# Kernel tuning notes

Hardware: AMD Instinct MI355X
Metric: run time of the kernel (lower is better)

Reference implementation:

```python
import jax, jax.numpy as jnp
import numpy as np

NUM_HEADS = 8
B, S, D = 4, 2048, 512


def setup_inputs() -> dict:
    key = jax.random.key(0)
    ks = jax.random.split(key, 12)
    scale = 1.0 / np.sqrt(D)
    return {
        "v": jax.random.normal(ks[0], (B, S, D), dtype=jnp.float32),
        "k": jax.random.normal(ks[1], (B, S, D), dtype=jnp.float32),
        "q": jax.random.normal(ks[2], (B, S, D), dtype=jnp.float32),
        "Wq": jax.random.normal(ks[3], (D, D), dtype=jnp.float32) * scale,
        "bq": jnp.zeros((D,), dtype=jnp.float32),
        "Wk": jax.random.normal(ks[4], (D, D), dtype=jnp.float32) * scale,
        "bk": jnp.zeros((D,), dtype=jnp.float32),
        "Wv": jax.random.normal(ks[5], (D, D), dtype=jnp.float32) * scale,
        "bv": jnp.zeros((D,), dtype=jnp.float32),
        "Wo": jax.random.normal(ks[6], (D, D), dtype=jnp.float32) * scale,
        "bo": jnp.zeros((D,), dtype=jnp.float32),
        "top_k": 32,
    }


def reference(v, k, q, Wq, bq, Wk, bk, Wv, bv, Wo, bo, top_k):
    dh = D // NUM_HEADS  # per-head depth

    def split_heads(x):  # [B,S,D] -> [B,H,S,dh]
        return x.reshape(B, -1, NUM_HEADS, dh).transpose(0, 2, 1, 3)

    qh = split_heads(q @ Wq + bq)
    kh = split_heads(k @ Wk + bk)
    vh = split_heads(v @ Wv + bv)

    logits = jnp.einsum('bhqd,bhkd->bhqk', qh, kh) / jnp.sqrt(jnp.float32(dh))
    w = jax.nn.softmax(logits, axis=-1)  # [B,H,S,S]

    num_keys = w.shape[-1]
    if top_k < num_keys:
        vals, idx = jax.lax.top_k(w, top_k)  # [B,H,S,top_k]
        bb = jnp.arange(B)[:, None, None, None]
        hh = jnp.arange(NUM_HEADS)[None, :, None, None]
        qq = jnp.arange(S)[None, None, :, None]
        sparse = jnp.zeros_like(w).at[bb, hh, qq, idx].set(vals)
        # tf.linalg.normalize(ord=1): divide by L1 norm along last axis
        w = sparse / jnp.sum(jnp.abs(sparse), axis=-1, keepdims=True)

    attn = jnp.einsum('bhqk,bhkd->bhqd', w, vh)  # [B,H,S,dh]
    concat = attn.transpose(0, 2, 1, 3).reshape(B, -1, D)
    out = concat @ Wo + bo
    return (out, w)
```

## Files before the change

kernel.cpp:

```cpp
#include <hip/hip_runtime.h>
#include <hip/hip_bf16.h>
#include <stdint.h>

#define S_LEN 2048
#define DMODEL 512
#define NH 8
#define DH 64
#define TOPK 32
#define LO_SCALE 4096.0f
#define INV_LO (1.0f/4096.0f)

typedef _Float16 f16;
typedef f16 half8 __attribute__((ext_vector_type(8)));
typedef f16 half4 __attribute__((ext_vector_type(4)));
typedef float floatx4 __attribute__((ext_vector_type(4)));
typedef float f32x4 __attribute__((ext_vector_type(4)));
typedef unsigned long long u64k;

#define AS1 __attribute__((address_space(1)))
#define AS3 __attribute__((address_space(3)))

__device__ __forceinline__ void gl_lds16(const void* g, void* l) {
    __builtin_amdgcn_global_load_lds((const AS1 void*)g, (AS3 void*)l, 16, 0, 0);
}
__device__ __forceinline__ void lds_fence() {
    asm volatile("s_waitcnt lgkmcnt(0)" ::: "memory");
}

__device__ __forceinline__ u64k make_key(float f, int idx) {
    unsigned u = __float_as_uint(f);
    unsigned sv = u ^ ((unsigned)(((int)u) >> 31) | 0x80000000u);
    return ((u64k)sv << 16) | (u64k)(0xFFFFu - (unsigned)idx);
}

__global__ __launch_bounds__(256)
void qkproj(const float* __restrict__ Xq, const float* __restrict__ Xk,
            const float* __restrict__ Wq_, const float* __restrict__ Wk_,
            const float* __restrict__ bq_, const float* __restrict__ bk_,
            float* __restrict__ outQ, float* __restrict__ outK)
{
    __shared__ float As[32][132];
    __shared__ float Bs[32][132];
    const float* X    = blockIdx.z ? Xk  : Xq;
    const float* W    = blockIdx.z ? Wk_ : Wq_;
    const float* bias = blockIdx.z ? bk_ : bq_;
    float* out        = blockIdx.z ? outK : outQ;
    const int tid = threadIdx.x;
    const int tx = tid & 15;
    const int ty = tid >> 4;
    const int m0 = blockIdx.y * 128;
    const int n0 = blockIdx.x * 128;

    float acc[8][8];
#pragma unroll
    for (int i = 0; i < 8; ++i)
#pragma unroll
        for (int j = 0; j < 8; ++j) acc[i][j] = 0.f;

    f32x4 pa[4], pb[4];
#pragma unroll
    for (int u = 0; u < 4; ++u) {
        int id = tid + u * 256;
        pa[u] = *(const f32x4*)(X + (size_t)(m0 + (id >> 3)) * 512 + (id & 7) * 4);
        pb[u] = *(const f32x4*)(W + (size_t)(id >> 5) * 512 + n0 + (id & 31) * 4);
    }

    for (int k0 = 0; k0 < 512; k0 += 32) {
#pragma unroll
        for (int u = 0; u < 4; ++u) {
            int id = tid + u * 256;
            int r = id >> 3, c4 = (id & 7) * 4;
            As[c4 + 0][r] = pa[u].x; As[c4 + 1][r] = pa[u].y;
            As[c4 + 2][r] = pa[u].z; As[c4 + 3][r] = pa[u].w;
            int rb = id >> 5, cb = (id & 31) * 4;
            *(f32x4*)&Bs[rb][cb] = pb[u];
        }
        __syncthreads();
        if (k0 < 480) {
            int kn = k0 + 32;
#pragma unroll
            for (int u = 0; u < 4; ++u) {
                int id = tid + u * 256;
                pa[u] = *(const f32x4*)(X + (size_t)(m0 + (id >> 3)) * 512 + kn + (id & 7) * 4);
                pb[u] = *(const f32x4*)(W + (size_t)(kn + (id >> 5)) * 512 + n0 + (id & 31) * 4);
            }
        }
#pragma unroll 8
        for (int kk = 0; kk < 32; ++kk) {
            float a[8], b[8];
            *(f32x4*)&a[0] = *(const f32x4*)&As[kk][ty * 4];
            *(f32x4*)&a[4] = *(const f32x4*)&As[kk][64 + ty * 4];
            *(f32x4*)&b[0] = *(const f32x4*)&Bs[kk][tx * 4];
            *(f32x4*)&b[4] = *(const f32x4*)&Bs[kk][64 + tx * 4];
#pragma unroll
            for (int i = 0; i < 8; ++i)
#pragma unroll
                for (int j = 0; j < 8; ++j)
                    acc[i][j] = fmaf(a[i], b[j], acc[i][j]);
        }
        __syncthreads();
    }

    float bb[8];
    *(f32x4*)&bb[0] = *(const f32x4*)(bias + n0 + tx * 4);
    *(f32x4*)&bb[4] = *(const f32x4*)(bias + n0 + 64 + tx * 4);

#pragma unroll
    for (int i = 0; i < 8; ++i) {
        int r = m0 + ((i >> 2) << 6) + ty * 4 + (i & 3);
        int b_ = r >> 11, s = r & 2047;
#pragma unroll
        for (int h = 0; h < 2; ++h) {
            int c = n0 + h * 64 + tx * 4;
            f32x4 w = {acc[i][h * 4 + 0] + bb[h * 4 + 0],
                       acc[i][h * 4 + 1] + bb[h * 4 + 1],
                       acc[i][h * 4 + 2] + bb[h * 4 + 2],
                       acc[i][h * 4 + 3] + bb[h * 4 + 3]};
            int hd = c >> 6, d = c & 63;
            float* p = out + (((size_t)(b_ * NH + hd) * S_LEN) + s) * DH + d;
            *(f32x4*)p = w;
        }
    }
}

__global__ __launch_bounds__(256)
void logits_topk(const float* __restrict__ Qh, const float* __restrict__ Kh,
                 float* __restrict__ wbuf)
{
    __shared__ float As[2][32][68];
    __shared__ __align__(16) char smemB[33280];
    float* Bs = (float*)smemB;
    u64k (*slab)[32] = (u64k(*)[32])smemB;

    const int tid = threadIdx.x;
    const int lig = tid & 15;
    const int ty  = tid >> 4;
    const int gsh = ((tid & 63) >> 4) << 4;
    const unsigned ltg = (1u << lig) - 1u;
    const int bh = blockIdx.y;
    const int q0 = blockIdx.x * 64;
    const float* Ab = Qh + (size_t)bh * S_LEN * DH;
    const float* Bb = Kh + (size_t)bh * S_LEN * DH;

    auto sort32 = [&](u64k &a0, u64k &a1) {
#pragma unroll
        for (int s = 2; s <= 32; s <<= 1) {
#pragma unroll
            for (int d = s >> 1; d >= 1; d >>= 1) {
                int e0 = 2 * lig;
                if (d == 1) {
                    bool descB = ((e0 & s) == 0);
                    u64k mx = a0 > a1 ? a0 : a1;
                    u64k mn = a0 > a1 ? a1 : a0;
                    a0 = descB ? mx : mn;
                    a1 = descB ? mn : mx;
                } else {
                    bool descB = ((e0 & s) == 0);
                    bool amS   = ((e0 & d) == 0);
                    bool wantMax = (descB == amS);
                    u64k p0 = __shfl_xor(a0, d >> 1, 16);
                    u64k p1 = __shfl_xor(a1, d >> 1, 16);
                    a0 = wantMax ? (a0 > p0 ? a0 : p0) : (a0 > p0 ? p0 : a0);
                    a1 = wantMax ? (a1 > p1 ? a1 : p1) : (a1 > p1 ? p1 : a1);
                }
            }
        }
    };
    auto clean32 = [&](u64k &a0, u64k &a1) {
#pragma unroll
        for (int d = 16; d >= 2; d >>= 1) {
            bool amS = (((2 * lig) & d) == 0);
            u64k p0 = __shfl_xor(a0, d >> 1, 16);
            u64k p1 = __shfl_xor(a1, d >> 1, 16);
            a0 = amS ? (a0 > p0 ? a0 : p0) : (a0 > p0 ? p0 : a0);
            a1 = amS ? (a1 > p1 ? a1 : p1) : (a1 > p1 ? p1 : a1);
        }
        u64k mx = a0 > a1 ? a0 : a1;
        u64k mn = a0 > a1 ? a1 : a0;
        a0 = mx; a1 = mn;
    };

    float acc[4][16];
#pragma unroll
    for (int i = 0; i < 4; ++i)
#pragma unroll
        for (int j = 0; j < 16; ++j) acc[i][j] = 0.f;

    u64k key0[4], key1[4], botk[4];
#pragma unroll
    for (int i = 0; i < 4; ++i) { key0[i] = 0; key1[i] = 0; botk[i] = 0; }

#pragma unroll
    for (int u = 0; u < 4; ++u) {
        int id = tid + u * 256;
        int r = id >> 4, c4 = (id & 15) * 4;
        int ch = c4 >> 5, cl = c4 & 31;
        f32x4 x = *(const f32x4*)(Ab + (size_t)(q0 + r) * DH + c4);
        As[ch][cl + 0][r] = x.x * 0.125f;
        As[ch][cl + 1][r] = x.y * 0.125f;
        As[ch][cl + 2][r] = x.z * 0.125f;
        As[ch][cl + 3][r] = x.w * 0.125f;
    }

    f32x4 kb[8];
#pragma unroll
    for (int u = 0; u < 8; ++u) {
        int id = tid + u * 256;
        int r = id >> 3, c4 = (id & 7) * 4;
        kb[u] = *(const f32x4*)(Bb + (size_t)r * DH + c4);
    }

#pragma unroll 1
    for (int kp = 0; kp < 8; ++kp) {
#pragma unroll
        for (int ch = 0; ch < 2; ++ch) {
            __syncthreads();
#pragma unroll
            for (int u = 0; u < 8; ++u) {
                int id = tid + u * 256;
                int r = id >> 3, c4 = (id & 7) * 4;
                Bs[(c4 + 0) * 260 + r] = kb[u].x;
                Bs[(c4 + 1) * 260 + r] = kb[u].y;
                Bs[(c4 + 2) * 260 + r] = kb[u].z;
                Bs[(c4 + 3) * 260 + r] = kb[u].w;
            }
            __syncthreads();
            {
                int nkp = ch ? kp + 1 : kp;
                int nch = ch ^ 1;
                if (nkp < 8) {
#pragma unroll
                    for (int u = 0; u < 8; ++u) {
                        int id = tid + u * 256;
                        int r = id >> 3, c4 = (id & 7) * 4;
                        kb[u] = *(const f32x4*)(Bb + (size_t)(nkp * 256 + r) * DH + nch * 32 + c4);
                    }
                }
            }
#pragma unroll 8
            for (int kk = 0; kk < 32; ++kk) {
                float a[4], b[16];
                *(f32x4*)&a[0] = *(const f32x4*)&As[ch][kk][ty * 4];
#pragma unroll
                for (int h = 0; h < 4; ++h)
                    *(f32x4*)&b[h * 4] = *(const f32x4*)&Bs[kk * 260 + lig * 4 + h * 64];
#pragma unroll
                for (int i = 0; i < 4; ++i)
#pragma unroll
                    for (int j = 0; j < 16; ++j)
                        acc[i][j] = fmaf(a[i], b[j], acc[i][j]);
            }
        }
        __syncthreads();

#pragma unroll
        for (int i = 0; i < 4; ++i) {
            unsigned done = 0;
            if (kp == 0) {
                u64k t0 = 0, t1 = 0; int j0 = 0, j1 = 0;
#pragma unroll
                for (int j = 0; j < 16; ++j) {
                    u64k kj = make_key(acc[i][j], ((j >> 2) << 6) + (lig << 2) + (j & 3));
                    if (kj > t0)      { t1 = t0; j1 = j0; t0 = kj; j0 = j; }
                    else if (kj > t1) { t1 = kj; j1 = j; }
                }
                key0[i] = t0; key1[i] = t1;
                sort32(key0[i], key1[i]);
                botk[i] = __shfl(key1[i], 15, 16);
                done = (1u << j0) | (1u << j1);
            }
            u64k bk = botk[i];
            int c = 0;
#pragma unroll 1
            for (int att = 0; att < 12; ++att) {
                bool ovf = false;
#pragma unroll
                for (int j = 0; j < 16; ++j) {
                    u64k kj = make_key(acc[i][j],
                                       kp * 256 + ((j >> 2) << 6) + (lig << 2) + (j & 3));
                    bool p = (((done >> j) & 1u) == 0u) && (kj > bk);
                    unsigned long long wbm = __ballot(p);
                    unsigned mk = (unsigned)((wbm >> gsh) & 0xFFFFull);
                    if (mk) {
                        int pos = c + __popc(mk & ltg);
                        int tot = c + __popc(mk);
                        if (p && pos < 32) { slab[ty * 4 + i][pos] = kj; done |= 1u << j; }
                        if (tot > 32) { ovf = true; c = 32; } else { c = tot; }
                    }
                }
                bool anyovf = __any(ovf);
                if (anyovf) {
                    lds_fence();
                    u64k c0 = (2 * lig     < c) ? slab[ty * 4 + i][2 * lig]     : 0ull;
                    u64k c1 = (2 * lig + 1 < c) ? slab[ty * 4 + i][2 * lig + 1] : 0ull;
                    sort32(c0, c1);
                    u64k m0 = __shfl_xor(c1, 15, 16);
                    u64k m1 = __shfl_xor(c0, 15, 16);
                    key0[i] = key0[i] > m0 ? key0[i] : m0;
                    key1[i] = key1[i] > m1 ? key1[i] : m1;
                    clean32(key0[i], key1[i]);
                    bk = __shfl(key1[i], 15, 16);
                    c = 0;
                } else {
                    break;
                }
            }
            {
                lds_fence();
                u64k c0 = (2 * lig     < c) ? slab[ty * 4 + i][2 * lig]     : 0ull;
                u64k c1 = (2 * lig + 1 < c) ? slab[ty * 4 + i][2 * lig + 1] : 0ull;
                sort32(c0, c1);
                u64k m0 = __shfl_xor(c1, 15, 16);
                u64k m1 = __shfl_xor(c0, 15, 16);
                key0[i] = key0[i] > m0 ? key0[i] : m0;
                key1[i] = key1[i] > m1 ? key1[i] : m1;
                clean32(key0[i], key1[i]);
                bk = __shfl(key1[i], 15, 16);
            }
            botk[i] = bk;
        }

#pragma unroll
        for (int i = 0; i < 4; ++i)
#pragma unroll
            for (int j = 0; j < 16; ++j) acc[i][j] = 0.f;
    }

#pragma unroll
    for (int i = 0; i < 4; ++i) {
        int r = q0 + ty * 4 + i;
        float* wr = wbuf + ((size_t)bh * S_LEN + r) * S_LEN;
        *(u64k*)(wr + (lig << 2))     = key0[i];
        *(u64k*)(wr + (lig << 2) + 2) = key1[i];
    }
}

__global__ __launch_bounds__(256)
void wsplit2(const float* __restrict__ W0, const float* __restrict__ W1,
             f16* __restrict__ planes)
{
    __shared__ float tile[32][33];
    const float* W = blockIdx.z ? W1 : W0;
    f16* Th = planes + (size_t)blockIdx.z * 524288;
    f16* Tl = Th + 262144;
    const int bx = blockIdx.x * 32;
    const int by = blockIdx.y * 32;
    const int lx = threadIdx.x & 31, ly = threadIdx.x >> 5;
#pragma unroll
    for (int r = ly; r < 32; r += 8)
        tile[r][lx] = W[(size_t)(by + r) * 512 + bx + lx];
    __syncthreads();
#pragma unroll
    for (int r = ly; r < 32; r += 8) {
        float x = tile[lx][r];
        f16 h = (f16)x;
        f16 l = (f16)((x - (float)h) * LO_SCALE);
        Th[(size_t)(bx + r) * 512 + by + lx] = h;
        Tl[(size_t)(bx + r) * 512 + by + lx] = l;
    }
}

__global__ __launch_bounds__(256)
void gemm_x32(const float* __restrict__ X,
              const f16* __restrict__ Bh_, const f16* __restrict__ Bl_,
              const float* __restrict__ bias, float* __restrict__ outF, int mode)
{
    __shared__ f16 sm[16384];
    f16* As_h = sm;       f16* As_l = sm + 4096;
    f16* Bs_h = sm + 8192; f16* Bs_l = sm + 12288;
    const int tid  = threadIdx.x;
    const int lane = tid & 63, wv = tid >> 6;
    const int wm = wv & 1, wn = wv >> 1;
    const int quad = lane >> 4, l15 = lane & 15;
    const int m0 = blockIdx.y * 128, n0 = blockIdx.x * 128;

    floatx4 acc_h[4][4], acc_c[4][4];
    const floatx4 z4 = {0.f, 0.f, 0.f, 0.f};
#pragma unroll
    for (int i = 0; i < 4; ++i)
#pragma unroll
        for (int j = 0; j < 4; ++j) { acc_h[i][j] = z4; acc_c[i][j] = z4; }

    for (int k0 = 0; k0 < 512; k0 += 32) {
        __syncthreads();
#pragma unroll
        for (int c = 0; c < 4; ++c) {
            int r   = c * 32 + (tid >> 3);
            int col = (tid & 7) * 4;
            f32x4 x = *(const f32x4*)(X + (size_t)(m0 + r) * 512 + k0 + col);
            f16 h0 = (f16)x.x, h1 = (f16)x.y, h2 = (f16)x.z, h3 = (f16)x.w;
            half4 hv = {h0, h1, h2, h3};
            half4 lv = {(f16)((x.x - (float)h0) * LO_SCALE),
                        (f16)((x.y - (float)h1) * LO_SCALE),
                        (f16)((x.z - (float)h2) * LO_SCALE),
                        (f16)((x.w - (float)h3) * LO_SCALE)};
            *(half4*)&As_h[r * 32 + col] = hv;
            *(half4*)&As_l[r * 32 + col] = lv;
        }
#pragma unroll
        for (int c = 0; c < 2; ++c) {
            int r    = c * 64 + (wv << 4) + (lane >> 2);
            int ch   = (lane & 3) * 8;
            int lidx = (c * 64 + (wv << 4)) * 32 + lane * 8;
            gl_lds16(Bh_ + (size_t)(n0 + r) * 512 + k0 + ch, &Bs_h[lidx]);
            gl_lds16(Bl_ + (size_t)(n0 + r) * 512 + k0 + ch, &Bs_l[lidx]);
        }
        asm volatile("s_waitcnt vmcnt(0)" ::: "memory");
        __syncthreads();

        half8 bh8[4], bl8[4];
#pragma unroll
        for (int j = 0; j < 4; ++j) {
            int n = wn * 64 + j * 16 + l15;
            bh8[j] = *(const half8*)&Bs_h[n * 32 + quad * 8];
            bl8[j] = *(const half8*)&Bs_l[n * 32 + quad * 8];
        }
#pragma unroll
        for (int i = 0; i < 4; ++i) {
            int m = wm * 64 + i * 16 + l15;
            half8 ah = *(const half8*)&As_h[m * 32 + quad * 8];
            half8 al = *(const half8*)&As_l[m * 32 + quad * 8];
#pragma unroll
            for (int j = 0; j < 4; ++j) {
                acc_h[i][j] = __builtin_amdgcn_mfma_f32_16x16x32_f16(ah, bh8[j], acc_h[i][j], 0, 0, 0);
                acc_c[i][j] = __builtin_amdgcn_mfma_f32_16x16x32_f16(ah, bl8[j], acc_c[i][j], 0, 0, 0);
                acc_c[i][j] = __builtin_amdgcn_mfma_f32_16x16x32_f16(al, bh8[j], acc_c[i][j], 0, 0, 0);
            }
        }
    }

#pragma unroll
    for (int j = 0; j < 4; ++j) {
        int col = n0 + wn * 64 + j * 16 + l15;
        float bv = bias[col];
#pragma unroll
        for (int i = 0; i < 4; ++i) {
            int rbase = m0 + wm * 64 + i * 16 + quad * 4;
#pragma unroll
            for (int rg = 0; rg < 4; ++rg) {
                float r = acc_h[i][j][rg] + acc_c[i][j][rg] * INV_LO + bv;
                int row = rbase + rg;
                if (mode == 2) {
                    outF[(size_t)row * 512 + col] = r;
                } else {
                    int b_ = row >> 11, s = row & 2047, h = col >> 6, d = col & 63;
                    outF[(((size_t)(b_ * NH + h)) * S_LEN + s) * DH + d] = r;
                }
            }
        }
    }
}

__global__ __launch_bounds__(256)
void gemm_x16(const f16* __restrict__ Ah_, const f16* __restrict__ Al_,
              const f16* __restrict__ Bh_, const f16* __restrict__ Bl_,
              const float* __restrict__ bias, float* __restrict__ outF,
              int Ksz, int ldc, int mode)
{
    __shared__ f16 sm[16384];
    f16* As_h = sm;        f16* As_l = sm + 4096;
    f16* Bs_h = sm + 8192; f16* Bs_l = sm + 12288;
    const int tid  = threadIdx.x;
    const int lane = tid & 63, wv = tid >> 6;
    const int wm = wv & 1, wn = wv >> 1;
    const int quad = lane >> 4, l15 = lane & 15;
    const int m0 = blockIdx.y * 128, n0 = blockIdx.x * 128;

    floatx4 acc_h[4][4], acc_c[4][4];
    const floatx4 z4 = {0.f, 0.f, 0.f, 0.f};
#pragma unroll
    for (int i = 0; i < 4; ++i)
#pragma unroll
        for (int j = 0; j < 4; ++j) { acc_h[i][j] = z4; acc_c[i][j] = z4; }

    for (int k0 = 0; k0 < Ksz; k0 += 32) {
        __syncthreads();
#pragma unroll
        for (int c = 0; c < 2; ++c) {
            int r    = c * 64 + (wv << 4) + (lane >> 2);
            int ch   = (lane & 3) * 8;
            int lidx = (c * 64 + (wv << 4)) * 32 + lane * 8;
            gl_lds16(Ah_ + (size_t)(m0 + r) * Ksz + k0 + ch, &As_h[lidx]);
            gl_lds16(Al_ + (size_t)(m0 + r) * Ksz + k0 + ch, &As_l[lidx]);
            gl_lds16(Bh_ + (size_t)(n0 + r) * Ksz + k0 + ch, &Bs_h[lidx]);
            gl_lds16(Bl_ + (size_t)(n0 + r) * Ksz + k0 + ch, &Bs_l[lidx]);
        }
        asm volatile("s_waitcnt vmcnt(0)" ::: "memory");
        __syncthreads();

        half8 bh8[4], bl8[4];
#pragma unroll
        for (int j = 0; j < 4; ++j) {
            int n = wn * 64 + j * 16 + l15;
            bh8[j] = *(const half8*)&Bs_h[n * 32 + quad * 8];
            bl8[j] = *(const half8*)&Bs_l[n * 32 + quad * 8];
        }
#pragma unroll
        for (int i = 0; i < 4; ++i) {
            int m = wm * 64 + i * 16 + l15;
            half8 ah = *(const half8*)&As_h[m * 32 + quad * 8];
            half8 al = *(const half8*)&As_l[m * 32 + quad * 8];
#pragma unroll
            for (int j = 0; j < 4; ++j) {
                acc_h[i][j] = __builtin_amdgcn_mfma_f32_16x16x32_f16(ah, bh8[j], acc_h[i][j], 0, 0, 0);
                acc_c[i][j] = __builtin_amdgcn_mfma_f32_16x16x32_f16(ah, bl8[j], acc_c[i][j], 0, 0, 0);
                acc_c[i][j] = __builtin_amdgcn_mfma_f32_16x16x32_f16(al, bh8[j], acc_c[i][j], 0, 0, 0);
            }
        }
    }

#pragma unroll
    for (int j = 0; j < 4; ++j) {
        int col = n0 + wn * 64 + j * 16 + l15;
        float bv = (mode == 2) ? bias[col] : 0.f;
#pragma unroll
        for (int i = 0; i < 4; ++i) {
            int rbase = m0 + wm * 64 + i * 16 + quad * 4;
#pragma unroll
            for (int rg = 0; rg < 4; ++rg) {
                float r = acc_h[i][j][rg] + acc_c[i][j][rg] * INV_LO;
                int row = rbase + rg;
                outF[(size_t)row * ldc + col] = r + bv;
            }
        }
    }
}

__global__ __launch_bounds__(256)
void topk_scatter(float* __restrict__ wbuf, const float* __restrict__ Vh,
                  f16* __restrict__ attH, f16* __restrict__ attL)
{
    __shared__ float wrow[4][2048];
    __shared__ float win_w[4][TOPK];
    __shared__ int   win_i[4][TOPK];

    const int tid  = threadIdx.x;
    const int wv   = tid >> 6;
    const int lane = tid & 63;
    const int row  = blockIdx.x * 4 + wv;
    float* wr = wbuf + (size_t)row * 2048;

    u64k key = 0;
    if (lane < TOPK) key = ((const u64k*)wr)[lane];
    unsigned sv = (unsigned)(key >> 16);
    unsigned fu = (sv & 0x80000000u) ? (sv ^ 0x80000000u) : ~sv;
    float v = __uint_as_float(fu);
    int idx = (int)(0xFFFFu - (unsigned)(key & 0xFFFFull)) & 2047;

    float m = __shfl(v, 0, 64);
    float e = (lane < TOPK) ? __expf(v - m) : 0.f;

    float mysum = e;
#pragma unroll
    for (int off = 32; off > 0; off >>= 1) mysum += __shfl_xor(mysum, off, 64);
    const float rw = 1.f / mysum;

    if (lane < TOPK) { win_w[wv][lane] = e; win_i[wv][lane] = idx; }

    const f32x4 z = {0.f, 0.f, 0.f, 0.f};
#pragma unroll
    for (int t = 0; t < 8; ++t) ((f32x4*)wrow[wv])[t * 64 + lane] = z;
    lds_fence();
    if (lane < TOPK) wrow[wv][win_i[wv][lane]] = win_w[wv][lane] * rw;
    lds_fence();

#pragma unroll
    for (int t = 0; t < 8; ++t)
        __builtin_nontemporal_store(((f32x4*)wrow[wv])[t * 64 + lane],
                                    (f32x4*)(wr + (size_t)(t * 64 + lane) * 4));

    const int bh = row >> 11;
    const float* Vb = Vh + (size_t)bh * S_LEN * DH;
    float acc = 0.f;
#pragma unroll
    for (int j = 0; j < TOPK; ++j) {
        float wj = win_w[wv][j] * rw;
        int   kj = win_i[wv][j];
        acc = fmaf(wj, Vb[(size_t)kj * DH + lane], acc);
    }
    const int b_ = row >> 14;
    const int h  = (row >> 11) & 7;
    const int s  = row & 2047;
    size_t oidx = (((size_t)b_ * S_LEN) + s) * 512 + h * DH + lane;
    f16 hh = (f16)acc;
    attH[oidx] = hh;
    attL[oidx] = (f16)((acc - (float)hh) * LO_SCALE);
}

extern "C" void kernel_launch(void* const* d_in, const int* in_sizes, int n_in,
                              void* d_out, int out_size, void* d_ws, size_t ws_size,
                              hipStream_t stream) {
    const float* v  = (const float*)d_in[0];
    const float* k  = (const float*)d_in[1];
    const float* q  = (const float*)d_in[2];
    const float* Wq = (const float*)d_in[3];
    const float* bq = (const float*)d_in[4];
    const float* Wk = (const float*)d_in[5];
    const float* bk = (const float*)d_in[6];
    const float* Wv = (const float*)d_in[7];
    const float* bv = (const float*)d_in[8];
    const float* Wo = (const float*)d_in[9];
    const float* bo = (const float*)d_in[10];

    float* out  = (float*)d_out;
    float* wout = out + (size_t)4 * S_LEN * 512;

    char* ws = (char*)d_ws;
    float* Vh   = (float*)ws;
    float* Qh32 = (float*)(ws + 16777216);
    float* Kh32 = (float*)(ws + 33554432);
    f16* WT  = (f16*)(ws + 50331648);
    f16 *WvH = WT,           *WvL = WT + 262144;
    f16 *WoH = WT + 524288,  *WoL = WT + 786432;
    f16* attH = (f16*)(ws + 16777216);
    f16* attL = (f16*)(ws + 25165824);

    wsplit2<<<dim3(16, 16, 2), 256, 0, stream>>>(Wv, Wo, WT);

    qkproj<<<dim3(4, 64, 2), 256, 0, stream>>>(q, k, Wq, Wk, bq, bk, Qh32, Kh32);
    gemm_x32<<<dim3(4, 64), 256, 0, stream>>>(v, WvH, WvL, bv, Vh, 1);

    logits_topk<<<dim3(32, 32), 256, 0, stream>>>(Qh32, Kh32, wout);

    topk_scatter<<<16384, 256, 0, stream>>>(wout, Vh, attH, attL);

    gemm_x16<<<dim3(4, 64, 1), 256, 0, stream>>>(attH, attL, WoH, WoL, bo, out, 512, 512, 2);
}
```

Baseline: 1.194 ms.

## Merge Q/K/V projections into one launch and double logits query tile

Q, K and V projections now run in a single kernel launch, with blockIdx.z choosing between the FP32 SIMT path and the split-f16 MFMA path. This removes one launch and lets the V GEMM overlap with the Q/K GEMMs. The logits_topk kernel now handles 128 query rows per block instead of 64, so each K tile loaded into LDS is reused across twice as many queries and the grid is halved. In exchange, the register prefetch of the next K chunk is dropped in favour of loading right before use. Register pressure also grows (acc[8][16] plus 8 rows of top-k keys), which risks spills or lower occupancy, and the grid shrinks to 512 blocks.

```diff
diff --git a/kernel.cpp b/kernel.cpp
--- a/kernel.cpp
+++ b/kernel.cpp
@@ -34,91 +34,178 @@
 }
 
 __global__ __launch_bounds__(256)
-void qkproj(const float* __restrict__ Xq, const float* __restrict__ Xk,
-            const float* __restrict__ Wq_, const float* __restrict__ Wk_,
-            const float* __restrict__ bq_, const float* __restrict__ bk_,
-            float* __restrict__ outQ, float* __restrict__ outK)
+void proj3(const float* __restrict__ Xq, const float* __restrict__ Xk,
+           const float* __restrict__ Xv,
+           const float* __restrict__ Wq_, const float* __restrict__ Wk_,
+           const f16* __restrict__ WvH, const f16* __restrict__ WvL,
+           const float* __restrict__ bq_, const float* __restrict__ bk_,
+           const float* __restrict__ bv_,
+           float* __restrict__ outQ, float* __restrict__ outK,
+           float* __restrict__ outV)
 {
-    __shared__ float As[32][132];
-    __shared__ float Bs[32][132];
-    const float* X    = blockIdx.z ? Xk  : Xq;
-    const float* W    = blockIdx.z ? Wk_ : Wq_;
-    const float* bias = blockIdx.z ? bk_ : bq_;
-    float* out        = blockIdx.z ? outK : outQ;
+    __shared__ __align__(16) char smem[33792];
     const int tid = threadIdx.x;
-    const int tx = tid & 15;
-    const int ty = tid >> 4;
     const int m0 = blockIdx.y * 128;
     const int n0 = blockIdx.x * 128;
 
-    float acc[8][8];
-#pragma unroll
-    for (int i = 0; i < 8; ++i)
-#pragma unroll
-        for (int j = 0; j < 8; ++j) acc[i][j] = 0.f;
-
-    f32x4 pa[4], pb[4];
-#pragma unroll
-    for (int u = 0; u < 4; ++u) {
-        int id = tid + u * 256;
-        pa[u] = *(const f32x4*)(X + (size_t)(m0 + (id >> 3)) * 512 + (id & 7) * 4);
-        pb[u] = *(const f32x4*)(W + (size_t)(id >> 5) * 512 + n0 + (id & 31) * 4);
-    }
-
-    for (int k0 = 0; k0 < 512; k0 += 32) {
+    if (blockIdx.z < 2) {
+        float (*As)[132] = (float(*)[132])smem;
+        float (*Bs)[132] = (float(*)[132])(smem + 16896);
+        const float* X    = blockIdx.z ? Xk  : Xq;
+        const float* W    = blockIdx.z ? Wk_ : Wq_;
+        const float* bias = blockIdx.z ? bk_ : bq_;
+        float* out        = blockIdx.z ? outK : outQ;
+        const int tx = tid & 15;
+        const int ty = tid >> 4;
+
+        float acc[8][8];
+#pragma unroll
+        for (int i = 0; i < 8; ++i)
+#pragma unroll
+            for (int j = 0; j < 8; ++j) acc[i][j] = 0.f;
+
+        f32x4 pa[4], pb[4];
 #pragma unroll
         for (int u = 0; u < 4; ++u) {
             int id = tid + u * 256;
-            int r = id >> 3, c4 = (id & 7) * 4;
-            As[c4 + 0][r] = pa[u].x; As[c4 + 1][r] = pa[u].y;
-            As[c4 + 2][r] = pa[u].z; As[c4 + 3][r] = pa[u].w;
-            int rb = id >> 5, cb = (id & 31) * 4;
-            *(f32x4*)&Bs[rb][cb] = pb[u];
-        }
-        __syncthreads();
-        if (k0 < 480) {
-            int kn = k0 + 32;
+            pa[u] = *(const f32x4*)(X + (size_t)(m0 + (id >> 3)) * 512 + (id & 7) * 4);
+            pb[u] = *(const f32x4*)(W + (size_t)(id >> 5) * 512 + n0 + (id & 31) * 4);
+        }
+
+        for (int k0 = 0; k0 < 512; k0 += 32) {
 #pragma unroll
             for (int u = 0; u < 4; ++u) {
                 int id = tid + u * 256;
-                pa[u] = *(const f32x4*)(X + (size_t)(m0 + (id >> 3)) * 512 + kn + (id & 7) * 4);
-                pb[u] = *(const f32x4*)(W + (size_t)(kn + (id >> 5)) * 512 + n0 + (id & 31) * 4);
-            }
-        }
+                int r = id >> 3, c4 = (id & 7) * 4;
+                As[c4 + 0][r] = pa[u].x; As[c4 + 1][r] = pa[u].y;
+                As[c4 + 2][r] = pa[u].z; As[c4 + 3][r] = pa[u].w;
+                int rb = id >> 5, cb = (id & 31) * 4;
+                *(f32x4*)&Bs[rb][cb] = pb[u];
+            }
+            __syncthreads();
+            if (k0 < 480) {
+                int kn = k0 + 32;
+#pragma unroll
+                for (int u = 0; u < 4; ++u) {
+                    int id = tid + u * 256;
+                    pa[u] = *(const f32x4*)(X + (size_t)(m0 + (id >> 3)) * 512 + kn + (id & 7) * 4);
+                    pb[u] = *(const f32x4*)(W + (size_t)(kn + (id >> 5)) * 512 + n0 + (id & 31) * 4);
+                }
+            }
 #pragma unroll 8
-        for (int kk = 0; kk < 32; ++kk) {
-            float a[8], b[8];
-            *(f32x4*)&a[0] = *(const f32x4*)&As[kk][ty * 4];
-            *(f32x4*)&a[4] = *(const f32x4*)&As[kk][64 + ty * 4];
-            *(f32x4*)&b[0] = *(const f32x4*)&Bs[kk][tx * 4];
-            *(f32x4*)&b[4] = *(const f32x4*)&Bs[kk][64 + tx * 4];
-#pragma unroll
-            for (int i = 0; i < 8; ++i)
-#pragma unroll
-                for (int j = 0; j < 8; ++j)
-                    acc[i][j] = fmaf(a[i], b[j], acc[i][j]);
-        }
-        __syncthreads();
-    }
-
-    float bb[8];
-    *(f32x4*)&bb[0] = *(const f32x4*)(bias + n0 + tx * 4);
-    *(f32x4*)&bb[4] = *(const f32x4*)(bias + n0 + 64 + tx * 4);
-
-#pragma unroll
-    for (int i = 0; i < 8; ++i) {
-        int r = m0 + ((i >> 2) << 6) + ty * 4 + (i & 3);
-        int b_ = r >> 11, s = r & 2047;
-#pragma unroll
-        for (int h = 0; h < 2; ++h) {
-            int c = n0 + h * 64 + tx * 4;
-            f32x4 w = {acc[i][h * 4 + 0] + bb[h * 4 + 0],
-                       acc[i][h * 4 + 1] + bb[h * 4 + 1],
-                       acc[i][h * 4 + 2] + bb[h * 4 + 2],
-                       acc[i][h * 4 + 3] + bb[h * 4 + 3]};
-            int hd = c >> 6, d = c & 63;
-            float* p = out + (((size_t)(b_ * NH + hd) * S_LEN) + s) * DH + d;
-            *(f32x4*)p = w;
+            for (int kk = 0; kk < 32; ++kk) {
+                float a[8], b[8];
+                *(f32x4*)&a[0] = *(const f32x4*)&As[kk][ty * 4];
+                *(f32x4*)&a[4] = *(const f32x4*)&As[kk][64 + ty * 4];
+                *(f32x4*)&b[0] = *(const f32x4*)&Bs[kk][tx * 4];
+                *(f32x4*)&b[4] = *(const f32x4*)&Bs[kk][64 + tx * 4];
+#pragma unroll
+                for (int i = 0; i < 8; ++i)
+#pragma unroll
+                    for (int j = 0; j < 8; ++j)
+                        acc[i][j] = fmaf(a[i], b[j], acc[i][j]);
+            }
+            __syncthreads();
+        }
+
+        float bb[8];
+        *(f32x4*)&bb[0] = *(const f32x4*)(bias + n0 + tx * 4);
+        *(f32x4*)&bb[4] = *(const f32x4*)(bias + n0 + 64 + tx * 4);
+
+#pragma unroll
+        for (int i = 0; i < 8; ++i) {
+            int r = m0 + ((i >> 2) << 6) + ty * 4 + (i & 3);
+            int b_ = r >> 11, s = r & 2047;
+#pragma unroll
+            for (int h = 0; h < 2; ++h) {
+                int c = n0 + h * 64 + tx * 4;
+                f32x4 w = {acc[i][h * 4 + 0] + bb[h * 4 + 0],
+                           acc[i][h * 4 + 1] + bb[h * 4 + 1],
+                           acc[i][h * 4 + 2] + bb[h * 4 + 2],
+                           acc[i][h * 4 + 3] + bb[h * 4 + 3]};
+                int hd = c >> 6, d = c & 63;
+                float* p = out + (((size_t)(b_ * NH + hd) * S_LEN) + s) * DH + d;
+                *(f32x4*)p = w;
+            }
+        }
+    } else {
+        f16* sm = (f16*)smem;
+        f16* As_h = sm;        f16* As_l = sm + 4096;
+        f16* Bs_h = sm + 8192; f16* Bs_l = sm + 12288;
+        const int lane = tid & 63, wv = tid >> 6;
+        const int wm = wv & 1, wn = wv >> 1;
+        const int quad = lane >> 4, l15 = lane & 15;
+
+        floatx4 acc_h[4][4], acc_c[4][4];
+        const floatx4 z4 = {0.f, 0.f, 0.f, 0.f};
+#pragma unroll
+        for (int i = 0; i < 4; ++i)
+#pragma unroll
+            for (int j = 0; j < 4; ++j) { acc_h[i][j] = z4; acc_c[i][j] = z4; }
+
+        for (int k0 = 0; k0 < 512; k0 += 32) {
+            __syncthreads();
+#pragma unroll
+            for (int c = 0; c < 4; ++c) {
+                int r   = c * 32 + (tid >> 3);
+                int col = (tid & 7) * 4;
+                f32x4 x = *(const f32x4*)(Xv + (size_t)(m0 + r) * 512 + k0 + col);
+                f16 h0 = (f16)x.x, h1 = (f16)x.y, h2 = (f16)x.z, h3 = (f16)x.w;
+                half4 hv = {h0, h1, h2, h3};
+                half4 lv = {(f16)((x.x - (float)h0) * LO_SCALE),
+                            (f16)((x.y - (float)h1) * LO_SCALE),
+                            (f16)((x.z - (float)h2) * LO_SCALE),
+                            (f16)((x.w - (float)h3) * LO_SCALE)};
+                *(half4*)&As_h[r * 32 + col] = hv;
+                *(half4*)&As_l[r * 32 + col] = lv;
+            }
+#pragma unroll
+            for (int c = 0; c < 2; ++c) {
+                int r    = c * 64 + (wv << 4) + (lane >> 2);
+                int ch   = (lane & 3) * 8;
+                int lidx = (c * 64 + (wv << 4)) * 32 + lane * 8;
+                gl_lds16(WvH + (size_t)(n0 + r) * 512 + k0 + ch, &Bs_h[lidx]);
+                gl_lds16(WvL + (size_t)(n0 + r) * 512 + k0 + ch, &Bs_l[lidx]);
+            }
+            asm volatile("s_waitcnt vmcnt(0)" ::: "memory");
+            __syncthreads();
+
+            half8 bh8[4], bl8[4];
+#pragma unroll
+            for (int j = 0; j < 4; ++j) {
+                int n = wn * 64 + j * 16 + l15;
+                bh8[j] = *(const half8*)&Bs_h[n * 32 + quad * 8];
+                bl8[j] = *(const half8*)&Bs_l[n * 32 + quad * 8];
+            }
+#pragma unroll
+            for (int i = 0; i < 4; ++i) {
+                int m = wm * 64 + i * 16 + l15;
+                half8 ah = *(const half8*)&As_h[m * 32 + quad * 8];
+                half8 al = *(const half8*)&As_l[m * 32 + quad * 8];
+#pragma unroll
+                for (int j = 0; j < 4; ++j) {
+                    acc_h[i][j] = __builtin_amdgcn_mfma_f32_16x16x32_f16(ah, bh8[j], acc_h[i][j], 0, 0, 0);
+                    acc_c[i][j] = __builtin_amdgcn_mfma_f32_16x16x32_f16(ah, bl8[j], acc_c[i][j], 0, 0, 0);
+                    acc_c[i][j] = __builtin_amdgcn_mfma_f32_16x16x32_f16(al, bh8[j], acc_c[i][j], 0, 0, 0);
+                }
+            }
+        }
+
+#pragma unroll
+        for (int j = 0; j < 4; ++j) {
+            int col = n0 + wn * 64 + j * 16 + l15;
+            float bv = bv_[col];
+#pragma unroll
+            for (int i = 0; i < 4; ++i) {
+                int rbase = m0 + wm * 64 + i * 16 + quad * 4;
+#pragma unroll
+                for (int rg = 0; rg < 4; ++rg) {
+                    float r = acc_h[i][j][rg] + acc_c[i][j][rg] * INV_LO + bv;
+                    int row = rbase + rg;
+                    int b_ = row >> 11, s = row & 2047, h = col >> 6, d = col & 63;
+                    outV[(((size_t)(b_ * NH + h)) * S_LEN + s) * DH + d] = r;
+                }
+            }
         }
     }
 }
@@ -127,7 +214,7 @@
 void logits_topk(const float* __restrict__ Qh, const float* __restrict__ Kh,
                  float* __restrict__ wbuf)
 {
-    __shared__ float As[2][32][68];
+    __shared__ float As[2][32][132];
     __shared__ __align__(16) char smemB[33280];
     float* Bs = (float*)smemB;
     u64k (*slab)[32] = (u64k(*)[32])smemB;
@@ -138,7 +225,7 @@
     const int gsh = ((tid & 63) >> 4) << 4;
     const unsigned ltg = (1u << lig) - 1u;
     const int bh = blockIdx.y;
-    const int q0 = blockIdx.x * 64;
+    const int q0 = blockIdx.x * 128;
     const float* Ab = Qh + (size_t)bh * S_LEN * DH;
     const float* Bb = Kh + (size_t)bh * S_LEN * DH;
 
@@ -180,18 +267,18 @@
         a0 = mx; a1 = mn;
     };
 
-    float acc[4][16];
-#pragma unroll
-    for (int i = 0; i < 4; ++i)
+    float acc[8][16];
+#pragma unroll
+    for (int i = 0; i < 8; ++i)
 #pragma unroll
         for (int j = 0; j < 16; ++j) acc[i][j] = 0.f;
 
-    u64k key0[4], key1[4], botk[4];
-#pragma unroll
-    for (int i = 0; i < 4; ++i) { key0[i] = 0; key1[i] = 0; botk[i] = 0; }
-
-#pragma unroll
-    for (int u = 0; u < 4; ++u) {
+    u64k key0[8], key1[8], botk[8];
+#pragma unroll
+    for (int i = 0; i < 8; ++i) { key0[i] = 0; key1[i] = 0; botk[i] = 0; }
+
+#pragma unroll
+    for (int u = 0; u < 8; ++u) {
         int id = tid + u * 256;
         int r = id >> 4, c4 = (id & 15) * 4;
         int ch = c4 >> 5, cl = c4 & 31;
@@ -202,18 +289,17 @@
         As[ch][cl + 3][r] = x.w * 0.125f;
     }
 
-    f32x4 kb[8];
-#pragma unroll
-    for (int u = 0; u < 8; ++u) {
-        int id = tid + u * 256;
-        int r = id >> 3, c4 = (id & 7) * 4;
-        kb[u] = *(const f32x4*)(Bb + (size_t)r * DH + c4);
-    }
-
 #pragma unroll 1
     for (int kp = 0; kp < 8; ++kp) {
 #pragma unroll
         for (int ch = 0; ch < 2; ++ch) {
+            f32x4 kb[8];
+#pragma unroll
+            for (int u = 0; u < 8; ++u) {
+                int id = tid + u * 256;
+                int r = id >> 3, c4 = (id & 7) * 4;
+                kb[u] = *(const f32x4*)(Bb + (size_t)(kp * 256 + r) * DH + ch * 32 + c4);
+            }
             __syncthreads();
 #pragma unroll
             for (int u = 0; u < 8; ++u) {
@@ -225,27 +311,16 @@
                 Bs[(c4 + 3) * 260 + r] = kb[u].w;
             }
             __syncthreads();
-            {
-                int nkp = ch ? kp + 1 : kp;
-                int nch = ch ^ 1;
-                if (nkp < 8) {
-#pragma unroll
-                    for (int u = 0; u < 8; ++u) {
-                        int id = tid + u * 256;
-                        int r = id >> 3, c4 = (id & 7) * 4;
-                        kb[u] = *(const f32x4*)(Bb + (size_t)(nkp * 256 + r) * DH + nch * 32 + c4);
-                    }
-                }
-            }
 #pragma unroll 8
             for (int kk = 0; kk < 32; ++kk) {
-                float a[4], b[16];
+                float a[8], b[16];
                 *(f32x4*)&a[0] = *(const f32x4*)&As[ch][kk][ty * 4];
+                *(f32x4*)&a[4] = *(const f32x4*)&As[ch][kk][64 + ty * 4];
 #pragma unroll
                 for (int h = 0; h < 4; ++h)
                     *(f32x4*)&b[h * 4] = *(const f32x4*)&Bs[kk * 260 + lig * 4 + h * 64];
 #pragma unroll
-                for (int i = 0; i < 4; ++i)
+                for (int i = 0; i < 8; ++i)
 #pragma unroll
                     for (int j = 0; j < 16; ++j)
                         acc[i][j] = fmaf(a[i], b[j], acc[i][j]);
@@ -254,7 +329,8 @@
         __syncthreads();
 
 #pragma unroll
-        for (int i = 0; i < 4; ++i) {
+        for (int i = 0; i < 8; ++i) {
+            const int rl = ((i >> 2) << 6) + ty * 4 + (i & 3);
             unsigned done = 0;
             if (kp == 0) {
                 u64k t0 = 0, t1 = 0; int j0 = 0, j1 = 0;
@@ -284,15 +360,15 @@
                     if (mk) {
                         int pos = c + __popc(mk & ltg);
                         int tot = c + __popc(mk);
-                        if (p && pos < 32) { slab[ty * 4 + i][pos] = kj; done |= 1u << j; }
+                        if (p && pos < 32) { slab[rl][pos] = kj; done |= 1u << j; }
                         if (tot > 32) { ovf = true; c = 32; } else { c = tot; }
                     }
                 }
                 bool anyovf = __any(ovf);
                 if (anyovf) {
                     lds_fence();
-                    u64k c0 = (2 * lig     < c) ? slab[ty * 4 + i][2 * lig]     : 0ull;
-                    u64k c1 = (2 * lig + 1 < c) ? slab[ty * 4 + i][2 * lig + 1] : 0ull;
+                    u64k c0 = (2 * lig     < c) ? slab[rl][2 * lig]     : 0ull;
+                    u64k c1 = (2 * lig + 1 < c) ? slab[rl][2 * lig + 1] : 0ull;
                     sort32(c0, c1);
                     u64k m0 = __shfl_xor(c1, 15, 16);
                     u64k m1 = __shfl_xor(c0, 15, 16);
@@ -307,8 +383,8 @@
             }
             {
                 lds_fence();
-                u64k c0 = (2 * lig     < c) ? slab[ty * 4 + i][2 * lig]     : 0ull;
-                u64k c1 = (2 * lig + 1 < c) ? slab[ty * 4 + i][2 * lig + 1] : 0ull;
+                u64k c0 = (2 * lig     < c) ? slab[rl][2 * lig]     : 0ull;
+                u64k c1 = (2 * lig + 1 < c) ? slab[rl][2 * lig + 1] : 0ull;
                 sort32(c0, c1);
                 u64k m0 = __shfl_xor(c1, 15, 16);
                 u64k m1 = __shfl_xor(c0, 15, 16);
@@ -321,14 +397,14 @@
         }
 
 #pragma unroll
-        for (int i = 0; i < 4; ++i)
+        for (int i = 0; i < 8; ++i)
 #pragma unroll
             for (int j = 0; j < 16; ++j) acc[i][j] = 0.f;
     }
 
 #pragma unroll
-    for (int i = 0; i < 4; ++i) {
-        int r = q0 + ty * 4 + i;
+    for (int i = 0; i < 8; ++i) {
+        int r = q0 + ((i >> 2) << 6) + ty * 4 + (i & 3);
         float* wr = wbuf + ((size_t)bh * S_LEN + r) * S_LEN;
         *(u64k*)(wr + (lig << 2))     = key0[i];
         *(u64k*)(wr + (lig << 2) + 2) = key1[i];
@@ -357,97 +433,6 @@
         f16 l = (f16)((x - (float)h) * LO_SCALE);
         Th[(size_t)(bx + r) * 512 + by + lx] = h;
         Tl[(size_t)(bx + r) * 512 + by + lx] = l;
-    }
-}
-
-__global__ __launch_bounds__(256)
-void gemm_x32(const float* __restrict__ X,
-              const f16* __restrict__ Bh_, const f16* __restrict__ Bl_,
-              const float* __restrict__ bias, float* __restrict__ outF, int mode)
-{
-    __shared__ f16 sm[16384];
-    f16* As_h = sm;       f16* As_l = sm + 4096;
-    f16* Bs_h = sm + 8192; f16* Bs_l = sm + 12288;
-    const int tid  = threadIdx.x;
-    const int lane = tid & 63, wv = tid >> 6;
-    const int wm = wv & 1, wn = wv >> 1;
-    const int quad = lane >> 4, l15 = lane & 15;
-    const int m0 = blockIdx.y * 128, n0 = blockIdx.x * 128;
-
-    floatx4 acc_h[4][4], acc_c[4][4];
-    const floatx4 z4 = {0.f, 0.f, 0.f, 0.f};
-#pragma unroll
-    for (int i = 0; i < 4; ++i)
-#pragma unroll
-        for (int j = 0; j < 4; ++j) { acc_h[i][j] = z4; acc_c[i][j] = z4; }
-
-    for (int k0 = 0; k0 < 512; k0 += 32) {
-        __syncthreads();
-#pragma unroll
-        for (int c = 0; c < 4; ++c) {
-            int r   = c * 32 + (tid >> 3);
-            int col = (tid & 7) * 4;
-            f32x4 x = *(const f32x4*)(X + (size_t)(m0 + r) * 512 + k0 + col);
-            f16 h0 = (f16)x.x, h1 = (f16)x.y, h2 = (f16)x.z, h3 = (f16)x.w;
-            half4 hv = {h0, h1, h2, h3};
-            half4 lv = {(f16)((x.x - (float)h0) * LO_SCALE),
-                        (f16)((x.y - (float)h1) * LO_SCALE),
-                        (f16)((x.z - (float)h2) * LO_SCALE),
-                        (f16)((x.w - (float)h3) * LO_SCALE)};
-            *(half4*)&As_h[r * 32 + col] = hv;
-            *(half4*)&As_l[r * 32 + col] = lv;
-        }
-#pragma unroll
-        for (int c = 0; c < 2; ++c) {
-            int r    = c * 64 + (wv << 4) + (lane >> 2);
-            int ch   = (lane & 3) * 8;
-            int lidx = (c * 64 + (wv << 4)) * 32 + lane * 8;
-            gl_lds16(Bh_ + (size_t)(n0 + r) * 512 + k0 + ch, &Bs_h[lidx]);
-            gl_lds16(Bl_ + (size_t)(n0 + r) * 512 + k0 + ch, &Bs_l[lidx]);
-        }
-        asm volatile("s_waitcnt vmcnt(0)" ::: "memory");
-        __syncthreads();
-
-        half8 bh8[4], bl8[4];
-#pragma unroll
-        for (int j = 0; j < 4; ++j) {
-            int n = wn * 64 + j * 16 + l15;
-            bh8[j] = *(const half8*)&Bs_h[n * 32 + quad * 8];
-            bl8[j] = *(const half8*)&Bs_l[n * 32 + quad * 8];
-        }
-#pragma unroll
-        for (int i = 0; i < 4; ++i) {
-            int m = wm * 64 + i * 16 + l15;
-            half8 ah = *(const half8*)&As_h[m * 32 + quad * 8];
-            half8 al = *(const half8*)&As_l[m * 32 + quad * 8];
-#pragma unroll
-            for (int j = 0; j < 4; ++j) {
-                acc_h[i][j] = __builtin_amdgcn_mfma_f32_16x16x32_f16(ah, bh8[j], acc_h[i][j], 0, 0, 0);
-                acc_c[i][j] = __builtin_amdgcn_mfma_f32_16x16x32_f16(ah, bl8[j], acc_c[i][j], 0, 0, 0);
-                acc_c[i][j] = __builtin_amdgcn_mfma_f32_16x16x32_f16(al, bh8[j], acc_c[i][j], 0, 0, 0);
-            }
-        }
-    }
-
-#pragma unroll
-    for (int j = 0; j < 4; ++j) {
-        int col = n0 + wn * 64 + j * 16 + l15;
-        float bv = bias[col];
-#pragma unroll
-        for (int i = 0; i < 4; ++i) {
-            int rbase = m0 + wm * 64 + i * 16 + quad * 4;
-#pragma unroll
-            for (int rg = 0; rg < 4; ++rg) {
-                float r = acc_h[i][j][rg] + acc_c[i][j][rg] * INV_LO + bv;
-                int row = rbase + rg;
-                if (mode == 2) {
-                    outF[(size_t)row * 512 + col] = r;
-                } else {
-                    int b_ = row >> 11, s = row & 2047, h = col >> 6, d = col & 63;
-                    outF[(((size_t)(b_ * NH + h)) * S_LEN + s) * DH + d] = r;
-                }
-            }
-        }
     }
 }
 
@@ -617,10 +602,10 @@
 
     wsplit2<<<dim3(16, 16, 2), 256, 0, stream>>>(Wv, Wo, WT);
 
-    qkproj<<<dim3(4, 64, 2), 256, 0, stream>>>(q, k, Wq, Wk, bq, bk, Qh32, Kh32);
-    gemm_x32<<<dim3(4, 64), 256, 0, stream>>>(v, WvH, WvL, bv, Vh, 1);
-
-    logits_topk<<<dim3(32, 32), 256, 0, stream>>>(Qh32, Kh32, wout);
+    proj3<<<dim3(4, 64, 3), 256, 0, stream>>>(q, k, v, Wq, Wk, WvH, WvL,
+                                              bq, bk, bv, Qh32, Kh32, Vh);
+
+    logits_topk<<<dim3(16, 32), 256, 0, stream>>>(Qh32, Kh32, wout);
 
     topk_scatter<<<16384, 256, 0, stream>>>(wout, Vh, attH, attL);
 
```

Measured after the change: 1.845 ms. 54.5% more time.
